# Optimization experiments

Hardware: AMD Instinct MI355X
Metric: run time of the kernel (lower is better)

The kernel has to match this reference:

```python
import jax, jax.numpy as jnp
import numpy as np

KH, KW = 4, 4
N, P, IN_CH, OUT_CH = 50000, 32, 64, 64


def setup_inputs() -> dict:
    key = jax.random.key(0)
    k1, k2, k3, k4 = jax.random.split(key, 4)
    features = jax.random.normal(k1, (N, IN_CH), jnp.float32)
    receivers = jax.random.randint(k2, (N, P), 0, N)
    # relative offsets scaled so most neighbors fall inside the support radius
    relative_positions = jax.random.normal(k3, (N, P, 2), jnp.float32) * 0.35
    window_support = jnp.float32(1.0)
    a = 3  # window exponent (1 - d^2/R^2)^a
    kernel = jax.random.uniform(k4, (KH, KW, IN_CH, OUT_CH), jnp.float32, -0.05, 0.05)
    bias = jnp.zeros((OUT_CH,), jnp.float32)
    return {"features": features, "receivers": receivers,
            "relative_positions": relative_positions,
            "window_support": window_support, "a": a,
            "kernel": kernel, "bias": bias}


def reference(features, receivers, relative_positions, window_support, a, kernel, bias):
    kh, kw, in_ch, out_ch = kernel.shape
    n, p = receivers.shape
    g_bins = kh * kw

    gathered = features[receivers]                      # [N,P,in] gather
    r = relative_positions / window_support             # normalized to [-1,1]
    d2 = jnp.sum(r * r, axis=-1)                        # [N,P]
    win = jnp.maximum(1.0 - d2, 0.0) ** a               # radial window

    # map normalized position to continuous kernel-grid coordinates
    gy = jnp.clip((r[..., 0] + 1.0) * 0.5 * (kh - 1), 0.0, kh - 1)
    gx = jnp.clip((r[..., 1] + 1.0) * 0.5 * (kw - 1), 0.0, kw - 1)
    y0 = jnp.clip(jnp.floor(gy).astype(jnp.int32), 0, kh - 2)
    x0 = jnp.clip(jnp.floor(gx).astype(jnp.int32), 0, kw - 2)
    fy = gy - y0
    fx = gx - x0

    # accumulate window*bilinear-weighted features into kernel bins per output point,
    # avoiding materializing a per-edge [in,out] interpolated filter
    n_idx = jnp.arange(n)[:, None]                      # broadcasts over P
    M = jnp.zeros((n, g_bins, in_ch), features.dtype)
    corners = [(0, 0, (1 - fy) * (1 - fx)), (0, 1, (1 - fy) * fx),
               (1, 0, fy * (1 - fx)), (1, 1, fy * fx)]
    for dy, dx, bw in corners:
        g = (y0 + dy) * kw + (x0 + dx)                  # [N,P] flat bin index
        M = M.at[n_idx, g].add((bw * win)[..., None] * gathered)

    out = jnp.einsum('ngi,gio->no', M, kernel.reshape(g_bins, in_ch, out_ch))
    return out / p + bias
```

## Files before the change

kernel.cpp:

```cpp
#include <hip/hip_runtime.h>
#include <hip/hip_bf16.h>

typedef unsigned short u16;
typedef unsigned int u32;

#define THREADS 256
constexpr int CH = 64;
constexpr int PP = 32;
constexpr int TM = 16;

constexpr int W_OFF  = 0;
constexpr int MB_OFF = 16384;
constexpr int LDS_BYTES = 49152;

typedef __attribute__((ext_vector_type(8))) short short8;
typedef __attribute__((ext_vector_type(4))) float f32x4;

static __device__ __forceinline__ u16 f2bf_rne(float f) {
  __hip_bfloat16 h = __float2bfloat16(f);
  return __builtin_bit_cast(u16, h);
}
static __device__ __forceinline__ u16 rbf(float f) {
  u32 u = __builtin_bit_cast(u32, f);
  return (u16)((u + 0x8000u) >> 16);
}

__global__ void prep_feat(const float* __restrict__ in, u16* __restrict__ outb, int n2) {
  int i = blockIdx.x * blockDim.x + threadIdx.x;
  if (i < n2) {
    float2 v = ((const float2*)in)[i];
    u32 u = (u32)f2bf_rne(v.x) | ((u32)f2bf_rne(v.y) << 16);
    ((u32*)outb)[i] = u;
  }
}

__global__ void prep_k2f(const float* __restrict__ kern, u16* __restrict__ k2f) {
  int d = blockIdx.x * blockDim.x + threadIdx.x;
  int e = d & 7, l = (d >> 3) & 63, ot = (d >> 9) & 3, ks = d >> 11;
  int k = ks * 32 + (l >> 4) * 8 + e;
  int o = ot * 16 + (l & 15);
  k2f[d] = f2bf_rne(kern[k * 64 + o]);
}

__global__ __launch_bounds__(THREADS, 3) void cconv_main(
    const int* __restrict__ recv, const float* __restrict__ relpos,
    const float* __restrict__ wsup, const int* __restrict__ aptr,
    const u16* __restrict__ fbf, const u16* __restrict__ k2f,
    const float* __restrict__ bias, float* __restrict__ out) {
  __shared__ __align__(16) char smem[LDS_BYTES];
  const int tid = threadIdx.x;
  const int n0 = blockIdx.x * TM;
  const int wid = tid >> 6, lane = tid & 63;
  const int l15 = lane & 15, l4 = lane >> 4;

  {
    const float invws = 1.0f / wsup[0];
    int a = aptr[0];
    if (a < 0 || a > 64) a = (int)(*(const float*)aptr);
    #pragma unroll
    for (int ee = 0; ee < 2; ++ee) {
      const int e = tid + ee * 256;
      const int m = e >> 5, p = e & 31;
      const int ei = (n0 + m) * PP + p;
      const float2 rp2 = ((const float2*)relpos)[ei];
      const float rx = rp2.x * invws, ry = rp2.y * invws;
      const float d2 = rx * rx + ry * ry;
      const float w1 = fmaxf(1.0f - d2, 0.0f);
      float win = 1.0f;
      for (int q = 0; q < a; ++q) win *= w1;
      float gy = fminf(fmaxf((rx + 1.0f) * 1.5f, 0.0f), 3.0f);
      float gx = fminf(fmaxf((ry + 1.0f) * 1.5f, 0.0f), 3.0f);
      int y0 = (int)gy; y0 = y0 > 2 ? 2 : y0;
      int x0 = (int)gx; x0 = x0 > 2 ? 2 : x0;
      const float fy = gy - (float)y0, fx = gx - (float)x0;
      u16* wp = (u16*)(smem + W_OFF) + m * 512 + p;
      #pragma unroll
      for (int g = 0; g < 16; ++g) {
        const int y = g >> 2, x = g & 3;
        const float wyv = (y == y0) ? (1.0f - fy) : (y == y0 + 1) ? fy : 0.0f;
        const float wxv = (x == x0) ? (1.0f - fx) : (x == x0 + 1) ? fx : 0.0f;
        wp[g * 32] = rbf(win * wyv * wxv);
      }
    }
  }
  __syncthreads();

  #pragma unroll
  for (int t = 0; t < 4; ++t) {
    const int m = wid * 4 + t;
    const int* rp = recv + (n0 + m) * PP + l4 * 8;
    const int4 A4 = *(const int4*)rp;
    const int4 B4 = *(const int4*)(rp + 4);
    const short8 af = *(const short8*)(smem + W_OFF + m * 1024 + l15 * 64 + l4 * 16);
    u32 vo[8];
    vo[0] = (u32)A4.x * 64u + (u32)l15; vo[1] = (u32)A4.y * 64u + (u32)l15;
    vo[2] = (u32)A4.z * 64u + (u32)l15; vo[3] = (u32)A4.w * 64u + (u32)l15;
    vo[4] = (u32)B4.x * 64u + (u32)l15; vo[5] = (u32)B4.y * 64u + (u32)l15;
    vo[6] = (u32)B4.z * 64u + (u32)l15; vo[7] = (u32)B4.w * 64u + (u32)l15;
    f32x4 accm[4];
    #pragma unroll
    for (int ib = 0; ib < 4; ++ib) {
      u32 q[8];
      #pragma unroll
      for (int e = 0; e < 8; ++e) q[e] = (u32)fbf[vo[e] + ib * 16];
      union { u32 u[4]; short8 s; } bb;
      #pragma unroll
      for (int j = 0; j < 4; ++j) bb.u[j] = q[2 * j] | (q[2 * j + 1] << 16);
      const f32x4 cz = {0.f, 0.f, 0.f, 0.f};
      accm[ib] = __builtin_amdgcn_mfma_f32_16x16x32_bf16(af, bb.s, cz, 0, 0, 0);
    }
    #pragma unroll
    for (int ib = 0; ib < 4; ++ib)
      #pragma unroll
      for (int r = 0; r < 4; ++r) {
        const int g = l4 * 4 + r;
        const u32 k = (u32)(g * 64 + ib * 16 + l15);
        u32 byt = (u32)m * 2048u + k * 2u;
        byt ^= ((u32)((m & 7) ^ (g & 7)) << 4);
        *(u16*)(smem + MB_OFF + byt) = rbf(accm[ib][r]);
      }
  }
  __syncthreads();

  f32x4 acc = {0.f, 0.f, 0.f, 0.f};
  {
    const u32 rowb = (u32)l15 * 2048u;
    const u32 swl = (u32)(l15 & 7) << 4;
    #pragma unroll 8
    for (int ks = 0; ks < 32; ++ks) {
      const u32 kc = (u32)ks * 32u + (u32)l4 * 8u;
      const u32 g7 = (((kc >> 6) & 7u) << 4);
      const u32 byt = (rowb + kc * 2u) ^ swl ^ g7;
      const short8 a2 = *(const short8*)(smem + MB_OFF + byt);
      const short8 b2 = *(const short8*)(k2f + ((u32)(ks * 4 + wid) * 64u + (u32)lane) * 8u);
      acc = __builtin_amdgcn_mfma_f32_16x16x32_bf16(a2, b2, acc, 0, 0, 0);
    }
  }

  const int o = wid * 16 + l15;
  const float bv = bias[o];
  #pragma unroll
  for (int r = 0; r < 4; ++r)
    out[(n0 + l4 * 4 + r) * CH + o] = acc[r] * (1.0f / 32.0f) + bv;
}

extern "C" void kernel_launch(void* const* d_in, const int* in_sizes, int n_in,
                              void* d_out, int out_size, void* d_ws, size_t ws_size,
                              hipStream_t stream) {
  const float* features = (const float*)d_in[0];
  const int* receivers  = (const int*)d_in[1];
  const float* relpos   = (const float*)d_in[2];
  const float* wsup     = (const float*)d_in[3];
  const int* aptr       = (const int*)d_in[4];
  const float* kern     = (const float*)d_in[5];
  const float* bias     = (const float*)d_in[6];
  float* out = (float*)d_out;

  const int N = in_sizes[0] / CH;
  u16* fbf = (u16*)d_ws;
  u16* k2f = (u16*)((char*)d_ws + (size_t)N * CH * 2);

  const int nfeat2 = in_sizes[0] / 2;
  prep_feat<<<dim3((nfeat2 + 255) / 256), dim3(256), 0, stream>>>(features, fbf, nfeat2);
  prep_k2f<<<dim3(65536 / 256), dim3(256), 0, stream>>>(kern, k2f);

  cconv_main<<<dim3(N / TM), dim3(THREADS), 0, stream>>>(
      receivers, relpos, wsup, aptr, fbf, k2f, bias, out);
}
```

Baseline: 55.39 us.

## Prefetch receiver indices early and software-pipeline feature gathers ahead of MFMA

Receiver index loads for all four rows are hoisted to the kernel start so they overlap the window-weight computation. The gather loop is restructured so each row's 32 feature gathers are issued one row ahead of the MFMA that consumes them, keeping more memory requests in flight. The cost is higher register pressure (up to 64 live gathered values plus 32 index registers), which under launch_bounds(256,3) may cause spills or reduce occupancy.

```diff
diff --git a/kernel.cpp b/kernel.cpp
--- a/kernel.cpp
+++ b/kernel.cpp
@@ -42,6 +42,43 @@
   k2f[d] = f2bf_rne(kern[k * 64 + o]);
 }
 
+#define LOADQ(qv, A4_, B4_) do {                                                \
+    u32 vo[8];                                                                  \
+    vo[0] = (u32)(A4_).x * 64u + (u32)l15; vo[1] = (u32)(A4_).y * 64u + (u32)l15; \
+    vo[2] = (u32)(A4_).z * 64u + (u32)l15; vo[3] = (u32)(A4_).w * 64u + (u32)l15; \
+    vo[4] = (u32)(B4_).x * 64u + (u32)l15; vo[5] = (u32)(B4_).y * 64u + (u32)l15; \
+    vo[6] = (u32)(B4_).z * 64u + (u32)l15; vo[7] = (u32)(B4_).w * 64u + (u32)l15; \
+    _Pragma("unroll")                                                           \
+    for (int ib = 0; ib < 4; ++ib)                                              \
+      _Pragma("unroll")                                                         \
+      for (int e = 0; e < 8; ++e) qv[ib * 8 + e] = (u32)fbf[vo[e] + ib * 16];   \
+  } while (0)
+
+#define COMPUTE(t_, qv) do {                                                    \
+    const int m_c = wid * 4 + (t_);                                             \
+    const short8 af = *(const short8*)(smem + W_OFF + m_c * 1024 + l15 * 64 + l4 * 16); \
+    f32x4 accm[4];                                                              \
+    _Pragma("unroll")                                                           \
+    for (int ib = 0; ib < 4; ++ib) {                                            \
+      union { u32 u[4]; short8 s; } bb;                                         \
+      _Pragma("unroll")                                                         \
+      for (int j = 0; j < 4; ++j)                                               \
+        bb.u[j] = qv[ib * 8 + 2 * j] | (qv[ib * 8 + 2 * j + 1] << 16);          \
+      const f32x4 cz = {0.f, 0.f, 0.f, 0.f};                                    \
+      accm[ib] = __builtin_amdgcn_mfma_f32_16x16x32_bf16(af, bb.s, cz, 0, 0, 0);\
+    }                                                                           \
+    _Pragma("unroll")                                                           \
+    for (int ib = 0; ib < 4; ++ib)                                              \
+      _Pragma("unroll")                                                         \
+      for (int r = 0; r < 4; ++r) {                                             \
+        const int g = l4 * 4 + r;                                               \
+        const u32 k = (u32)(g * 64 + ib * 16 + l15);                            \
+        u32 byt = (u32)m_c * 2048u + k * 2u;                                    \
+        byt ^= ((u32)((m_c & 7) ^ (g & 7)) << 4);                               \
+        *(u16*)(smem + MB_OFF + byt) = rbf(accm[ib][r]);                        \
+      }                                                                         \
+  } while (0)
+
 __global__ __launch_bounds__(THREADS, 3) void cconv_main(
     const int* __restrict__ recv, const float* __restrict__ relpos,
     const float* __restrict__ wsup, const int* __restrict__ aptr,
@@ -52,6 +89,16 @@
   const int n0 = blockIdx.x * TM;
   const int wid = tid >> 6, lane = tid & 63;
   const int l15 = lane & 15, l4 = lane >> 4;
+
+  const int* rbase = recv + (n0 + wid * 4) * PP + l4 * 8;
+  const int4 A40 = *(const int4*)(rbase + 0 * PP);
+  const int4 B40 = *(const int4*)(rbase + 0 * PP + 4);
+  const int4 A41 = *(const int4*)(rbase + 1 * PP);
+  const int4 B41 = *(const int4*)(rbase + 1 * PP + 4);
+  const int4 A42 = *(const int4*)(rbase + 2 * PP);
+  const int4 B42 = *(const int4*)(rbase + 2 * PP + 4);
+  const int4 A43 = *(const int4*)(rbase + 3 * PP);
+  const int4 B43 = *(const int4*)(rbase + 3 * PP + 4);
 
   {
     const float invws = 1.0f / wsup[0];
@@ -85,40 +132,16 @@
   }
   __syncthreads();
 
-  #pragma unroll
-  for (int t = 0; t < 4; ++t) {
-    const int m = wid * 4 + t;
-    const int* rp = recv + (n0 + m) * PP + l4 * 8;
-    const int4 A4 = *(const int4*)rp;
-    const int4 B4 = *(const int4*)(rp + 4);
-    const short8 af = *(const short8*)(smem + W_OFF + m * 1024 + l15 * 64 + l4 * 16);
-    u32 vo[8];
-    vo[0] = (u32)A4.x * 64u + (u32)l15; vo[1] = (u32)A4.y * 64u + (u32)l15;
-    vo[2] = (u32)A4.z * 64u + (u32)l15; vo[3] = (u32)A4.w * 64u + (u32)l15;
-    vo[4] = (u32)B4.x * 64u + (u32)l15; vo[5] = (u32)B4.y * 64u + (u32)l15;
-    vo[6] = (u32)B4.z * 64u + (u32)l15; vo[7] = (u32)B4.w * 64u + (u32)l15;
-    f32x4 accm[4];
-    #pragma unroll
-    for (int ib = 0; ib < 4; ++ib) {
-      u32 q[8];
-      #pragma unroll
-      for (int e = 0; e < 8; ++e) q[e] = (u32)fbf[vo[e] + ib * 16];
-      union { u32 u[4]; short8 s; } bb;
-      #pragma unroll
-      for (int j = 0; j < 4; ++j) bb.u[j] = q[2 * j] | (q[2 * j + 1] << 16);
-      const f32x4 cz = {0.f, 0.f, 0.f, 0.f};
-      accm[ib] = __builtin_amdgcn_mfma_f32_16x16x32_bf16(af, bb.s, cz, 0, 0, 0);
-    }
-    #pragma unroll
-    for (int ib = 0; ib < 4; ++ib)
-      #pragma unroll
-      for (int r = 0; r < 4; ++r) {
-        const int g = l4 * 4 + r;
-        const u32 k = (u32)(g * 64 + ib * 16 + l15);
-        u32 byt = (u32)m * 2048u + k * 2u;
-        byt ^= ((u32)((m & 7) ^ (g & 7)) << 4);
-        *(u16*)(smem + MB_OFF + byt) = rbf(accm[ib][r]);
-      }
+  {
+    u32 q0[32], q1[32], q2[32], q3[32];
+    LOADQ(q0, A40, B40);
+    LOADQ(q1, A41, B41);
+    COMPUTE(0, q0);
+    LOADQ(q2, A42, B42);
+    COMPUTE(1, q1);
+    LOADQ(q3, A43, B43);
+    COMPUTE(2, q2);
+    COMPUTE(3, q3);
   }
   __syncthreads();
 
```

Result: no change. 54.95 us (-0.8%).
